# Kernel tuning notes

Measured on AMD Instinct MI355X. Metric: run time of the kernel, lower is better.

## Reference

```python
import jax, jax.numpy as jnp
import numpy as np

R = 32          # voxel_resolution
GN_GROUPS = 8   # GroupNorm groups used throughout the module


def group_norm(x, scale, bias, groups, eps=1e-5):
    B, C = x.shape[0], x.shape[1]
    spatial = x.shape[2:]
    xg = x.reshape(B, groups, C // groups, -1)
    mu = xg.mean(axis=(2, 3), keepdims=True)
    var = xg.var(axis=(2, 3), keepdims=True)
    xn = ((xg - mu) / jnp.sqrt(var + eps)).reshape((B, C) + spatial)
    sh = (1, C) + (1,) * len(spatial)
    return xn * scale.reshape(sh) + bias.reshape(sh)


def conv3d_same(x, w, b):
    pad = w.shape[-1] // 2
    y = jax.lax.conv_general_dilated(
        x, w, (1, 1, 1), [(pad, pad)] * 3,
        dimension_numbers=('NCDHW', 'OIDHW', 'NCDHW'))
    return y + b.reshape(1, -1, 1, 1, 1)


def _voxelize(coords, features, r):
    # PVCNN Voxelization: center coords, normalize to [0,1], scale to grid,
    # scatter-MEAN point features into a dense [B,C,r,r,r] grid.
    B, C, N = features.shape
    centered = coords - coords.mean(axis=2, keepdims=True)            # [B,3,N]
    norm = jnp.linalg.norm(centered, axis=1, keepdims=True)           # [B,1,N]
    denom = norm.max(axis=2, keepdims=True) * 2.0                     # eps = 0
    nc = centered / denom + 0.5
    nc = jnp.clip(nc * r, 0.0, r - 1.0)                               # float voxel coords
    vi = jnp.round(nc).astype(jnp.int32)                              # [B,3,N]
    flat = (vi[:, 0] * r + vi[:, 1]) * r + vi[:, 2]                   # [B,N]
    seg = (flat + (jnp.arange(B, dtype=jnp.int32) * (r ** 3))[:, None]).reshape(-1)
    feats = features.transpose(0, 2, 1).reshape(B * N, C)
    sums = jax.ops.segment_sum(feats, seg, num_segments=B * r ** 3)
    cnts = jax.ops.segment_sum(jnp.ones((B * N,), feats.dtype), seg,
                               num_segments=B * r ** 3)
    mean = sums / jnp.maximum(cnts, 1.0)[:, None]
    grid = mean.reshape(B, r, r, r, C).transpose(0, 4, 1, 2, 3)       # [B,C,r,r,r]
    return nc, grid


def _trilinear_devoxelize(nc, grid, r):
    # nc [B,3,N] float in [0,r-1]; grid [B,C,r,r,r] -> gather 8 corners + weights
    B, C = grid.shape[0], grid.shape[1]
    lo = jnp.floor(nc)
    frac = nc - lo                                                    # [B,3,N]
    lo_i = lo.astype(jnp.int32)
    hi_i = jnp.minimum(lo_i + 1, r - 1)
    gf = grid.reshape(B, C, r * r * r)
    out = jnp.zeros((B, C, nc.shape[2]), grid.dtype)
    for dx in (0, 1):
        for dy in (0, 1):
            for dz in (0, 1):
                ix = hi_i[:, 0] if dx else lo_i[:, 0]
                iy = hi_i[:, 1] if dy else lo_i[:, 1]
                iz = hi_i[:, 2] if dz else lo_i[:, 2]
                w = ((frac[:, 0] if dx else 1.0 - frac[:, 0]) *
                     (frac[:, 1] if dy else 1.0 - frac[:, 1]) *
                     (frac[:, 2] if dz else 1.0 - frac[:, 2]))        # [B,N]
                idx = (ix * r + iy) * r + iz                          # [B,N]
                g = jnp.take_along_axis(gf, idx[:, None, :], axis=2)  # [B,C,N]
                out = out + g * w[:, None, :]
    return out


def setup_inputs() -> dict:
    key = jax.random.key(0)
    ks = jax.random.split(key, 6)
    B, N, Cin, Cout, K = 4, 65536, 64, 128, 3
    return {
        'coords':   jax.random.normal(ks[0], (B, 3, N), jnp.float32),
        'features': jax.random.normal(ks[1], (B, Cin, N), jnp.float32),
        'conv1_w':  jax.random.normal(ks[2], (Cout, Cin, K, K, K), jnp.float32) * 0.02,
        'conv1_b':  jnp.zeros((Cout,), jnp.float32),
        'gn1_scale': jnp.ones((Cout,), jnp.float32),
        'gn1_bias':  jnp.zeros((Cout,), jnp.float32),
        'conv2_w':  jax.random.normal(ks[3], (Cout, Cout, K, K, K), jnp.float32) * 0.02,
        'conv2_b':  jnp.zeros((Cout,), jnp.float32),
        'gn2_scale': jnp.ones((Cout,), jnp.float32),
        'gn2_bias':  jnp.zeros((Cout,), jnp.float32),
        'point_w':  jax.random.normal(ks[4], (Cout, Cin), jnp.float32) * 0.05,
        'point_b':  jnp.zeros((Cout,), jnp.float32),
        'point_gn_scale': jnp.ones((Cout,), jnp.float32),
        'point_gn_bias':  jnp.zeros((Cout,), jnp.float32),
    }


def reference(coords, features, conv1_w, conv1_b, gn1_scale, gn1_bias,
              conv2_w, conv2_b, gn2_scale, gn2_bias,
              point_w, point_b, point_gn_scale, point_gn_bias):
    nc, grid = _voxelize(coords, features, R)
    # voxel branch: Conv3d -> GN -> SiLU -> (dropout, eval: identity) -> Conv3d -> GN -> SiLU
    h = conv3d_same(grid, conv1_w, conv1_b)
    h = jax.nn.silu(group_norm(h, gn1_scale, gn1_bias, GN_GROUPS))
    h = conv3d_same(h, conv2_w, conv2_b)
    h = jax.nn.silu(group_norm(h, gn2_scale, gn2_bias, GN_GROUPS))
    # point branch: SharedMLP = 1x1 Conv1d -> GN -> SiLU
    p = jnp.einsum('oc,bcn->bon', point_w, features) + point_b[None, :, None]
    p = jax.nn.silu(group_norm(p, point_gn_scale, point_gn_bias, GN_GROUPS))
    vpts = _trilinear_devoxelize(nc, h, R)                            # [B,Cout,N]
    return p + vpts
```

## Files before the change

### kernel.cpp

```cpp
#include <hip/hip_runtime.h>

typedef __attribute__((ext_vector_type(8))) short bf16x8;
typedef __attribute__((ext_vector_type(4))) float f32x4;
typedef __attribute__((ext_vector_type(4))) int i32x4;
typedef __attribute__((ext_vector_type(2))) int i32x2;

#define B_ 4
#define N_ 65536
#define RRR_ 32768
#define PADV_ 39304
#define PPLANE_ 1156

static const size_t OFF_NC     = 0;
static const size_t OFF_VIDX   = 786432;
static const size_t OFF_WT1    = 1048576;
static const size_t OFF_WT2    = 1159168;
static const size_t OFF_C2OUT  = 1380352;
static const size_t OFF_CNT    = 9768960;
static const size_t OFF_GSUM   = 9900032;
static const size_t OFF_GPAD   = 18288640;
static const size_t OFF_ACT1   = 23319552;
static const size_t OFF_GSTATS = 33381376;
static const size_t OFF_BSTATS = 33381568;
static const size_t MEMSET_FLOATS = 33381584 - 9768960;
static const size_t OFF_PBF    = 9900032;

__device__ __forceinline__ ushort f2bf(float x) {
    union { float f; unsigned u; } c; c.f = x;
    unsigned r = c.u + 0x7fffu + ((c.u >> 16) & 1u);
    return (ushort)(r >> 16);
}
__device__ __forceinline__ float bf2f(ushort h) {
    union { unsigned u; float f; } c; c.u = ((unsigned)h) << 16;
    return c.f;
}

__device__ __forceinline__ void gl16(const void* g, void* l) {
    __builtin_amdgcn_global_load_lds(
        (const __attribute__((address_space(1))) unsigned int*)(g),
        (__attribute__((address_space(3))) unsigned int*)(l),
        16, 0, 0);
}

__global__ __launch_bounds__(256) void k_coord_sum(const float* __restrict__ coords,
                                                   float* __restrict__ bstats) {
    int b = blockIdx.y;
    int tid = threadIdx.x;
    const float* cb = coords + (size_t)b * 3 * N_;
    float s0 = 0.f, s1 = 0.f, s2 = 0.f;
    for (int n = blockIdx.x * 256 + tid; n < N_; n += 64 * 256) {
        s0 += cb[n]; s1 += cb[N_ + n]; s2 += cb[2 * N_ + n];
    }
    #pragma unroll
    for (int off = 1; off < 64; off <<= 1) {
        s0 += __shfl_xor(s0, off);
        s1 += __shfl_xor(s1, off);
        s2 += __shfl_xor(s2, off);
    }
    if ((tid & 63) == 0) {
        atomicAdd(&bstats[b * 4 + 0], s0);
        atomicAdd(&bstats[b * 4 + 1], s1);
        atomicAdd(&bstats[b * 4 + 2], s2);
    }
}

__global__ __launch_bounds__(256) void k_coord_max(const float* __restrict__ coords,
                                                   float* __restrict__ bstats) {
    int b = blockIdx.y;
    int tid = threadIdx.x;
    const float invN = 1.0f / (float)N_;
    float m0 = bstats[b * 4 + 0] * invN;
    float m1 = bstats[b * 4 + 1] * invN;
    float m2 = bstats[b * 4 + 2] * invN;
    const float* cb = coords + (size_t)b * 3 * N_;
    float mx = 0.f;
    for (int n = blockIdx.x * 256 + tid; n < N_; n += 64 * 256) {
        float x = cb[n] - m0, y = cb[N_ + n] - m1, z = cb[2 * N_ + n] - m2;
        mx = fmaxf(mx, x * x + y * y + z * z);
    }
    #pragma unroll
    for (int off = 1; off < 64; off <<= 1)
        mx = fmaxf(mx, __shfl_xor(mx, off));
    if ((tid & 63) == 0)
        atomicMax((int*)&bstats[b * 4 + 3], __float_as_int(mx));
}

__global__ __launch_bounds__(256) void k_point_prep(const float* __restrict__ coords,
                                                    const float* __restrict__ bstats,
                                                    float* __restrict__ nc,
                                                    int* __restrict__ vidx,
                                                    float* __restrict__ cnt) {
    int gid = blockIdx.x * 256 + threadIdx.x;
    int b = gid >> 16;
    int n = gid & (N_ - 1);
    const float invN = 1.0f / (float)N_;
    float m[3] = {bstats[b * 4 + 0] * invN, bstats[b * 4 + 1] * invN, bstats[b * 4 + 2] * invN};
    float den = 2.0f * sqrtf(__int_as_float(((const int*)bstats)[b * 4 + 3]));
    const float* cb = coords + (size_t)b * 3 * N_;
    int vi[3];
    #pragma unroll
    for (int d = 0; d < 3; ++d) {
        float cv = cb[(size_t)d * N_ + n];
        float t = (cv - m[d]) / den + 0.5f;
        t *= 32.0f;
        t = fminf(fmaxf(t, 0.0f), 31.0f);
        nc[((size_t)b * 3 + d) * N_ + n] = t;
        vi[d] = (int)rintf(t);
    }
    int flat = (vi[0] * 32 + vi[1]) * 32 + vi[2];
    vidx[(b << 16) + n] = flat;
    atomicAdd(&cnt[(b << 15) + flat], 1.0f);
}

__global__ __launch_bounds__(256) void k_scatter_cl(const float* __restrict__ feats,
                                                    const int* __restrict__ vidx,
                                                    float* __restrict__ gsum) {
    __shared__ float lf[64 * 129];
    __shared__ int sidx[128];
    int tid = threadIdx.x;
    int b = blockIdx.y;
    int n0 = blockIdx.x * 128;
    for (int i = tid; i < 64 * 128; i += 256) {
        int ci = i >> 7, pt = i & 127;
        lf[ci * 129 + pt] = feats[((size_t)(b * 64 + ci)) * N_ + n0 + pt];
    }
    if (tid < 128) sidx[tid] = vidx[(b << 16) + n0 + tid];
    __syncthreads();
    for (int i = tid; i < 64 * 128; i += 256) {
        int ci = i & 63, pt = i >> 6;
        atomicAdd(&gsum[((size_t)(b << 15) + sidx[pt]) * 64 + ci], lf[ci * 129 + pt]);
    }
}

__global__ __launch_bounds__(256) void k_gridmean_cl(const float* __restrict__ gsum,
                                                     const float* __restrict__ cnt,
                                                     ushort* __restrict__ gpad) {
    int idx = blockIdx.x * 256 + threadIdx.x;
    int q = idx & 15;
    int vox = (idx >> 4) & 32767;
    int b = idx >> 19;
    float c = cnt[(b << 15) + vox];
    float inv = 1.0f / fmaxf(c, 1.0f);
    float4 v = *(const float4*)(gsum + (((size_t)(b << 15) + vox) << 6) + q * 4);
    int zz = vox >> 10, yy = (vox >> 5) & 31, xx = vox & 31;
    size_t o = ((size_t)b * PADV_ + (size_t)(zz + 1) * PPLANE_ + (yy + 1) * 34 + (xx + 1)) * 64 + q * 4;
    i32x2 pk;
    ushort* u = (ushort*)&pk;
    u[0] = f2bf(v.x * inv); u[1] = f2bf(v.y * inv);
    u[2] = f2bf(v.z * inv); u[3] = f2bf(v.w * inv);
    *(i32x2*)(gpad + o) = pk;
}

template <int CI>
__global__ __launch_bounds__(256) void k_wtrans(const float* __restrict__ w,
                                                ushort* __restrict__ wt) {
    int idx = blockIdx.x * 256 + threadIdx.x;
    if (idx >= 27 * 128 * CI) return;
    int chin = idx & 31;
    int co = (idx >> 5) & 127;
    int t3 = idx >> 12;
    int tap = t3 % 27;
    int chunk = t3 / 27;
    int ci = chunk * 32 + chin;
    wt[idx] = f2bf(w[((size_t)co * CI + ci) * 27 + tap]);
}

template <int CI, bool PAD_OUT>
__global__ __launch_bounds__(256, 3) void k_conv(const ushort* __restrict__ inp,
                                                 const ushort* __restrict__ wt,
                                                 const float* __restrict__ bias,
                                                 ushort* __restrict__ outp,
                                                 float* __restrict__ gstats,
                                                 int layer) {
    constexpr int NCHUNK = CI / 32;
    __shared__ char lds[40960];

    const int bid = blockIdx.x;
    const int wid = (bid & 7) * 128 + (bid >> 3);
    const int yg = wid & 7;
    const int z0 = (wid >> 3) & 31;
    const int b = wid >> 8;
    const int y0 = yg * 4;
    const int tid = threadIdx.x;
    const int w = tid >> 6, l = tid & 63;
    const int lk = l >> 4, lr = l & 15;
    const int wr = w >> 1, wc = w & 1;

    const char* actb = (const char*)(inp + (size_t)b * PADV_ * CI);
    const char* wtb = (const char*)wt;

    int st_glb[10];
    #pragma unroll
    for (int j = 0; j < 10; ++j) {
        int c = j * 64 + (tid >> 2);
        if (c > 611) c = 611;
        int row = c / 34;
        int x = c - row * 34;
        int dz = row / 6, dy = row - dz * 6;
        int gz = z0 + dz, gy = y0 + dy;
        int lq = (tid & 3) ^ ((x >> 1) & 3);
        st_glb[j] = (gz * PPLANE_ + gy * 34 + x) * CI * 2 + lq * 16;
    }

    int aoff[4][3];
    #pragma unroll
    for (int i = 0; i < 4; ++i) {
        int pos = wr * 64 + i * 16 + lr;
        int ly = pos >> 5, x = pos & 31;
        #pragma unroll
        for (int fx = 0; fx < 3; ++fx) {
            int xc = x + fx;
            aoff[i][fx] = (ly * 34 + xc) * 64 + ((lk ^ ((xc >> 1) & 3)) << 4);
        }
    }
    int bln[4];
    #pragma unroll
    for (int n = 0; n < 4; ++n)
        bln[n] = ((wc * 64 + n * 16 + lr) * 32 + lk * 8) * 2;

    f32x4 acc[4][4];
    #pragma unroll
    for (int i = 0; i < 4; ++i)
        #pragma unroll
        for (int n = 0; n < 4; ++n)
            acc[i][n] = (f32x4){0.f, 0.f, 0.f, 0.f};

    #pragma unroll 1
    for (int chunk = 0; chunk < NCHUNK; ++chunk) {
        __syncthreads();
        const char* wchunk = wtb + (size_t)chunk * 27 * 8192;
        bf16x8 bq[4][4];
        #pragma unroll
        for (int tp = 0; tp < 4; ++tp)
            #pragma unroll
            for (int n = 0; n < 4; ++n)
                bq[tp][n] = *(const bf16x8*)(wchunk + tp * 8192 + bln[n]);
        {
            const char* srcb = actb + chunk * 64;
            #pragma unroll
            for (int j = 0; j < 10; ++j)
                gl16(srcb + st_glb[j], lds + j * 4096 + w * 1024);
        }
        __syncthreads();

        #pragma unroll
        for (int t = 0; t < 27; ++t) {
            const int fz = t / 9, r9v = t - fz * 9;
            const int fy = r9v / 3, fx = r9v - fy * 3;
            const int drow = (fz * 6 + fy) * 2176;
            bf16x8 af[4];
            #pragma unroll
            for (int i = 0; i < 4; ++i)
                af[i] = *(const bf16x8*)(lds + drow + aoff[i][fx]);
            #pragma unroll
            for (int i = 0; i < 4; ++i)
                #pragma unroll
                for (int n = 0; n < 4; ++n)
                    acc[i][n] = __builtin_amdgcn_mfma_f32_16x16x32_bf16(af[i], bq[t & 3][n], acc[i][n], 0, 0, 0);
            if (t + 4 < 27) {
                const char* wp = wchunk + (size_t)(t + 4) * 8192;
                #pragma unroll
                for (int n = 0; n < 4; ++n) bq[t & 3][n] = *(const bf16x8*)(wp + bln[n]);
            }
        }
    }

    __syncthreads();
    ushort* outs = (ushort*)lds;
    float bb[4];
    #pragma unroll
    for (int n = 0; n < 4; ++n) bb[n] = bias[wc * 64 + n * 16 + lr];
    float sg[4] = {0.f, 0.f, 0.f, 0.f}, sq[4] = {0.f, 0.f, 0.f, 0.f};
    #pragma unroll
    for (int i = 0; i < 4; ++i) {
        int posb = wr * 64 + i * 16 + lk * 4;
        #pragma unroll
        for (int n = 0; n < 4; ++n) {
            int co = wc * 64 + n * 16 + lr;
            #pragma unroll
            for (int r = 0; r < 4; ++r) {
                float v = acc[i][n][r] + bb[n];
                sg[n] += v; sq[n] += v * v;
                outs[(posb + r) * 128 + co] = f2bf(v);
            }
        }
    }
    #pragma unroll
    for (int off = 1; off < 64; off <<= 1) {
        #pragma unroll
        for (int n = 0; n < 4; ++n) {
            sg[n] += __shfl_xor(sg[n], off);
            sq[n] += __shfl_xor(sq[n], off);
        }
    }
    if (l == 0) {
        int gbase = layer * 32 + b * 8 + wc * 4;
        #pragma unroll
        for (int n = 0; n < 4; ++n) {
            atomicAdd(&gstats[(gbase + n) * 2 + 0], sg[n]);
            atomicAdd(&gstats[(gbase + n) * 2 + 1], sq[n]);
        }
    }
    __syncthreads();
    for (int idx = tid; idx < 2048; idx += 256) {
        int pos = idx >> 4, c8 = idx & 15;
        int yy = y0 + (pos >> 5), xx = pos & 31;
        size_t g;
        if (PAD_OUT)
            g = ((size_t)b * PADV_ + (size_t)(z0 + 1) * PPLANE_ + (yy + 1) * 34 + (xx + 1)) * 128 + c8 * 8;
        else
            g = ((size_t)b * RRR_ + z0 * 1024 + yy * 32 + xx) * 128 + c8 * 8;
        *(i32x4*)(outp + g) = *((i32x4*)lds + idx);
    }
}

template <bool PAD>
__global__ __launch_bounds__(256) void k_gn_apply(ushort* __restrict__ x,
                                                  const float* __restrict__ gstats,
                                                  const float* __restrict__ sc,
                                                  const float* __restrict__ bi,
                                                  int layer, float invc) {
    int idx = blockIdx.x * 256 + threadIdx.x;
    int c8 = idx & 15;
    int vox = (idx >> 4) & 32767;
    int b = idx >> 19;
    size_t base;
    if (PAD) {
        int zz = vox >> 10, yy = (vox >> 5) & 31, xx = vox & 31;
        base = ((size_t)b * PADV_ + (size_t)(zz + 1) * PPLANE_ + (yy + 1) * 34 + (xx + 1)) * 128 + c8 * 8;
    } else {
        base = ((size_t)b * RRR_ + vox) * 128 + c8 * 8;
    }
    int g = c8 >> 1;
    float sum = gstats[(layer * 32 + b * 8 + g) * 2 + 0];
    float ssq = gstats[(layer * 32 + b * 8 + g) * 2 + 1];
    float mean = sum * invc;
    float var = ssq * invc - mean * mean;
    float rstd = rsqrtf(var + 1e-5f);
    i32x4 raw = *(i32x4*)(x + base);
    ushort* u = (ushort*)&raw;
    #pragma unroll
    for (int j = 0; j < 8; ++j) {
        int co = c8 * 8 + j;
        float v = bf2f(u[j]);
        v = (v - mean) * rstd * sc[co] + bi[co];
        v = v / (1.f + __expf(-v));
        u[j] = f2bf(v);
    }
    *(i32x4*)(x + base) = raw;
}

__global__ __launch_bounds__(256) void k_point_mlp(const float* __restrict__ feats,
                                                   const float* __restrict__ w,
                                                   const float* __restrict__ pb,
                                                   ushort* __restrict__ pbf,
                                                   float* __restrict__ gstats) {
    __shared__ float wl[64 * 132];
    __shared__ float sred[4][16];
    int tid = threadIdx.x;
    for (int i = tid; i < 128 * 64; i += 256) {
        int o = i >> 6, c = i & 63;
        wl[c * 132 + o] = w[i];
    }
    __syncthreads();
    int gid = blockIdx.x * 256 + tid;
    int b = gid >> 16, n = gid & (N_ - 1);
    const float* fb = feats + (size_t)b * 64 * N_ + n;
    float acc[128];
    #pragma unroll
    for (int o = 0; o < 128; ++o) acc[o] = 0.f;
    for (int c = 0; c < 64; ++c) {
        float f = fb[(size_t)c * N_];
        const float4* wr4 = (const float4*)&wl[c * 132];
        #pragma unroll
        for (int o4 = 0; o4 < 32; ++o4) {
            float4 wv = wr4[o4];
            acc[4 * o4 + 0] = fmaf(f, wv.x, acc[4 * o4 + 0]);
            acc[4 * o4 + 1] = fmaf(f, wv.y, acc[4 * o4 + 1]);
            acc[4 * o4 + 2] = fmaf(f, wv.z, acc[4 * o4 + 2]);
            acc[4 * o4 + 3] = fmaf(f, wv.w, acc[4 * o4 + 3]);
        }
    }
    ushort* ob = pbf + (size_t)b * 128 * N_ + n;
    float sg[8] = {0.f}, sq[8] = {0.f};
    #pragma unroll
    for (int o = 0; o < 128; ++o) {
        float v = acc[o] + pb[o];
        ob[(size_t)o * N_] = f2bf(v);
        sg[o >> 4] += v;
        sq[o >> 4] += v * v;
    }
    #pragma unroll
    for (int off = 1; off < 64; off <<= 1) {
        #pragma unroll
        for (int g = 0; g < 8; ++g) {
            sg[g] += __shfl_xor(sg[g], off);
            sq[g] += __shfl_xor(sq[g], off);
        }
    }
    int wv = tid >> 6, l = tid & 63;
    if (l == 0) {
        #pragma unroll
        for (int g = 0; g < 8; ++g) { sred[wv][g] = sg[g]; sred[wv][8 + g] = sq[g]; }
    }
    __syncthreads();
    if (tid < 16) {
        float v = sred[0][tid] + sred[1][tid] + sred[2][tid] + sred[3][tid];
        int g = tid & 7, part = tid >> 3;
        atomicAdd(&gstats[(64 + b * 8 + g) * 2 + part], v);
    }
}

__global__ __launch_bounds__(256) void k_devox_final(const float* __restrict__ nc,
                                                     const ushort* __restrict__ ht,
                                                     const ushort* __restrict__ pbf,
                                                     const float* __restrict__ gstats,
                                                     const float* __restrict__ scale,
                                                     const float* __restrict__ bias,
                                                     float* __restrict__ out) {
    __shared__ float vp[64][129];
    __shared__ int sidx[64][8];
    __shared__ float swt[64][8];
    int tid = threadIdx.x;
    int blk = blockIdx.x;
    int b = blk >> 10;
    int n0 = (blk & 1023) * 64;
    if (tid < 64) {
        int n = n0 + tid;
        float f0 = nc[(size_t)b * 3 * N_ + n];
        float f1 = nc[((size_t)b * 3 + 1) * N_ + n];
        float f2 = nc[((size_t)b * 3 + 2) * N_ + n];
        float l0 = floorf(f0), l1 = floorf(f1), l2 = floorf(f2);
        float r0 = f0 - l0, r1 = f1 - l1, r2 = f2 - l2;
        int i0 = (int)l0, i1 = (int)l1, i2 = (int)l2;
        int h0 = min(i0 + 1, 31), h1 = min(i1 + 1, 31), h2 = min(i2 + 1, 31);
        #pragma unroll
        for (int k = 0; k < 8; ++k) {
            int dx = (k >> 2) & 1, dy = (k >> 1) & 1, dz = k & 1;
            int ix = dx ? h0 : i0, iy = dy ? h1 : i1, iz = dz ? h2 : i2;
            float w = (dx ? r0 : 1.f - r0) * (dy ? r1 : 1.f - r1) * (dz ? r2 : 1.f - r2);
            sidx[tid][k] = (ix * 32 + iy) * 32 + iz;
            swt[tid][k] = w;
        }
    }
    __syncthreads();
    const ushort* hb = ht + (size_t)b * RRR_ * 128;
    for (int t = tid; t < 64 * 16; t += 256) {
        int c8 = t & 15, pt = t >> 4;
        float a[8] = {0.f, 0.f, 0.f, 0.f, 0.f, 0.f, 0.f, 0.f};
        #pragma unroll
        for (int k = 0; k < 8; ++k) {
            i32x4 raw = *(const i32x4*)(hb + (size_t)sidx[pt][k] * 128 + c8 * 8);
            ushort* u = (ushort*)&raw;
            float wk = swt[pt][k];
            #pragma unroll
            for (int j = 0; j < 8; ++j)
                a[j] = fmaf(wk, bf2f(u[j]), a[j]);
        }
        #pragma unroll
        for (int j = 0; j < 8; ++j)
            vp[pt][c8 * 8 + j] = a[j];
    }
    __syncthreads();
    const float invc = 1.0f / (16.0f * (float)N_);
    for (int t = tid; t < 64 * 128; t += 256) {
        int nl = t & 63;
        int c = t >> 6;
        int g = c >> 4;
        float sum = gstats[(64 + b * 8 + g) * 2 + 0];
        float ssq = gstats[(64 + b * 8 + g) * 2 + 1];
        float mean = sum * invc;
        float var = ssq * invc - mean * mean;
        float rstd = rsqrtf(var + 1e-5f);
        size_t o = ((size_t)(b * 128 + c)) * N_ + n0 + nl;
        float v = (bf2f(pbf[o]) - mean) * rstd * scale[c] + bias[c];
        v = v / (1.f + __expf(-v));
        out[o] = v + vp[nl][c];
    }
}

extern "C" void kernel_launch(void* const* d_in, const int* in_sizes, int n_in,
                              void* d_out, int out_size, void* d_ws, size_t ws_size,
                              hipStream_t stream) {
    const float* coords   = (const float*)d_in[0];
    const float* features = (const float*)d_in[1];
    const float* conv1_w  = (const float*)d_in[2];
    const float* conv1_b  = (const float*)d_in[3];
    const float* gn1_s    = (const float*)d_in[4];
    const float* gn1_b    = (const float*)d_in[5];
    const float* conv2_w  = (const float*)d_in[6];
    const float* conv2_b  = (const float*)d_in[7];
    const float* gn2_s    = (const float*)d_in[8];
    const float* gn2_b    = (const float*)d_in[9];
    const float* point_w  = (const float*)d_in[10];
    const float* point_b  = (const float*)d_in[11];
    const float* pgn_s    = (const float*)d_in[12];
    const float* pgn_b    = (const float*)d_in[13];
    float* out = (float*)d_out;
    float* ws = (float*)d_ws;

    float*  nc     = ws + OFF_NC;
    int*    vidx   = (int*)(ws + OFF_VIDX);
    ushort* wt1    = (ushort*)(ws + OFF_WT1);
    ushort* wt2    = (ushort*)(ws + OFF_WT2);
    ushort* c2out  = (ushort*)(ws + OFF_C2OUT);
    float*  cnt    = ws + OFF_CNT;
    float*  gsum   = ws + OFF_GSUM;
    ushort* gpad   = (ushort*)(ws + OFF_GPAD);
    ushort* act1   = (ushort*)(ws + OFF_ACT1);
    float*  gstats = ws + OFF_GSTATS;
    float*  bstats = ws + OFF_BSTATS;
    ushort* pbf    = (ushort*)(ws + OFF_PBF);

    const float invc = 1.0f / (float)(RRR_ * 16);

    hipMemsetAsync(cnt, 0, MEMSET_FLOATS * sizeof(float), stream);

    k_coord_sum<<<dim3(64, B_), 256, 0, stream>>>(coords, bstats);
    k_coord_max<<<dim3(64, B_), 256, 0, stream>>>(coords, bstats);
    k_point_prep<<<B_ * N_ / 256, 256, 0, stream>>>(coords, bstats, nc, vidx, cnt);
    k_scatter_cl<<<dim3(N_ / 128, B_), 256, 0, stream>>>(features, vidx, gsum);
    k_gridmean_cl<<<B_ * RRR_ * 16 / 256, 256, 0, stream>>>(gsum, cnt, gpad);

    k_wtrans<64><<<(27 * 128 * 64 + 255) / 256, 256, 0, stream>>>(conv1_w, wt1);
    k_wtrans<128><<<(27 * 128 * 128 + 255) / 256, 256, 0, stream>>>(conv2_w, wt2);

    k_conv<64, true><<<1024, 256, 0, stream>>>(gpad, wt1, conv1_b, act1, gstats, 0);
    k_gn_apply<true><<<B_ * RRR_ * 16 / 256, 256, 0, stream>>>(act1, gstats, gn1_s, gn1_b, 0, invc);

    k_conv<128, false><<<1024, 256, 0, stream>>>(act1, wt2, conv2_b, c2out, gstats, 1);
    k_gn_apply<false><<<B_ * RRR_ * 16 / 256, 256, 0, stream>>>(c2out, gstats, gn2_s, gn2_b, 1, invc);

    k_point_mlp<<<B_ * N_ / 256, 256, 0, stream>>>(features, point_w, point_b, pbf, gstats);
    k_devox_final<<<B_ * N_ / 64, 256, 0, stream>>>(nc, c2out, pbf, gstats, pgn_s, pgn_b, out);
}
```

Baseline: 1.036 ms.

## Stream conv weight taps through a swizzled LDS double-buffer ring with async loads

The conv kernel stops loading per-tap weight fragments from global memory into registers four taps ahead. Instead it stages each tap's weights into a two-slot LDS ring with async global-to-LDS copies, paced by explicit vmcnt waits and barriers, and uses setprio around the MFMA block. This is meant to cut register pressure and redundant global weight reads across waves, at the cost of more LDS, two barriers per tap and a lower occupancy hint (3 to 2). The devox kernel also remaps its block index to interleave batches.

Result: faster. 936.5 us (-9.6%).

```diff
diff --git a/kernel.cpp b/kernel.cpp
--- a/kernel.cpp
+++ b/kernel.cpp
@@ -166,14 +166,15 @@
 }
 
 template <int CI, bool PAD_OUT>
-__global__ __launch_bounds__(256, 3) void k_conv(const ushort* __restrict__ inp,
+__global__ __launch_bounds__(256, 2) void k_conv(const ushort* __restrict__ inp,
                                                  const ushort* __restrict__ wt,
                                                  const float* __restrict__ bias,
                                                  ushort* __restrict__ outp,
                                                  float* __restrict__ gstats,
                                                  int layer) {
     constexpr int NCHUNK = CI / 32;
-    __shared__ char lds[40960];
+    __shared__ char lds[40960 + 16384];
+    char* ring = lds + 40960;
 
     const int bid = blockIdx.x;
     const int wid = (bid & 7) * 128 + (bid >> 3);
@@ -201,7 +202,14 @@
         int lq = (tid & 3) ^ ((x >> 1) & 3);
         st_glb[j] = (gz * PPLANE_ + gy * 34 + x) * CI * 2 + lq * 16;
     }
-
+    int bst[2];
+    #pragma unroll
+    for (int i = 0; i < 2; ++i) {
+        int s = tid + i * 256;
+        int q = s & 3, co = s >> 2;
+        int sco = (co & 3) ^ ((co >> 2) & 3);
+        bst[i] = co * 64 + ((q ^ sco) << 4);
+    }
     int aoff[4][3];
     #pragma unroll
     for (int i = 0; i < 4; ++i) {
@@ -213,10 +221,13 @@
             aoff[i][fx] = (ly * 34 + xc) * 64 + ((lk ^ ((xc >> 1) & 3)) << 4);
         }
     }
-    int bln[4];
-    #pragma unroll
-    for (int n = 0; n < 4; ++n)
-        bln[n] = ((wc * 64 + n * 16 + lr) * 32 + lk * 8) * 2;
+    int boff[4];
+    #pragma unroll
+    for (int n = 0; n < 4; ++n) {
+        int co = wc * 64 + n * 16 + lr;
+        int sco = (co & 3) ^ ((co >> 2) & 3);
+        boff[n] = co * 64 + ((lk ^ sco) << 4);
+    }
 
     f32x4 acc[4][4];
     #pragma unroll
@@ -227,45 +238,60 @@
 
     #pragma unroll 1
     for (int chunk = 0; chunk < NCHUNK; ++chunk) {
-        __syncthreads();
-        const char* wchunk = wtb + (size_t)chunk * 27 * 8192;
-        bf16x8 bq[4][4];
-        #pragma unroll
-        for (int tp = 0; tp < 4; ++tp)
-            #pragma unroll
-            for (int n = 0; n < 4; ++n)
-                bq[tp][n] = *(const bf16x8*)(wchunk + tp * 8192 + bln[n]);
-        {
-            const char* srcb = actb + chunk * 64;
-            #pragma unroll
-            for (int j = 0; j < 10; ++j)
-                gl16(srcb + st_glb[j], lds + j * 4096 + w * 1024);
-        }
-        __syncthreads();
+        const char* srcb = actb + chunk * 64;
+        const char* wch = wtb + (size_t)chunk * 27 * 8192;
+        #pragma unroll
+        for (int j = 0; j < 10; ++j)
+            gl16(srcb + st_glb[j], lds + j * 4096 + w * 1024);
+        #pragma unroll
+        for (int i = 0; i < 2; ++i)
+            gl16(wch + bst[i], ring + i * 4096 + w * 1024);
+        #pragma unroll
+        for (int i = 0; i < 2; ++i)
+            gl16(wch + 8192 + bst[i], ring + 8192 + i * 4096 + w * 1024);
 
         #pragma unroll
         for (int t = 0; t < 27; ++t) {
+            __builtin_amdgcn_sched_barrier(0);
+            if (t == 26) {
+                asm volatile("s_waitcnt vmcnt(0)" ::: "memory");
+            } else {
+                asm volatile("s_waitcnt vmcnt(2)" ::: "memory");
+            }
+            __builtin_amdgcn_sched_barrier(0);
+            __builtin_amdgcn_s_barrier();
+            __builtin_amdgcn_sched_barrier(0);
+            const char* rp = ring + (t & 1) * 8192;
             const int fz = t / 9, r9v = t - fz * 9;
             const int fy = r9v / 3, fx = r9v - fy * 3;
             const int drow = (fz * 6 + fy) * 2176;
-            bf16x8 af[4];
+            bf16x8 af[4], bfr[4];
             #pragma unroll
             for (int i = 0; i < 4; ++i)
                 af[i] = *(const bf16x8*)(lds + drow + aoff[i][fx]);
             #pragma unroll
+            for (int n = 0; n < 4; ++n)
+                bfr[n] = *(const bf16x8*)(rp + boff[n]);
+            __builtin_amdgcn_s_setprio(1);
+            #pragma unroll
             for (int i = 0; i < 4; ++i)
                 #pragma unroll
                 for (int n = 0; n < 4; ++n)
-                    acc[i][n] = __builtin_amdgcn_mfma_f32_16x16x32_bf16(af[i], bq[t & 3][n], acc[i][n], 0, 0, 0);
-            if (t + 4 < 27) {
-                const char* wp = wchunk + (size_t)(t + 4) * 8192;
+                    acc[i][n] = __builtin_amdgcn_mfma_f32_16x16x32_bf16(af[i], bfr[n], acc[i][n], 0, 0, 0);
+            __builtin_amdgcn_s_setprio(0);
+            __builtin_amdgcn_sched_barrier(0);
+            __builtin_amdgcn_s_barrier();
+            __builtin_amdgcn_sched_barrier(0);
+            if (t + 2 < 27) {
+                const char* wp = wch + (size_t)(t + 2) * 8192;
+                char* rw = ring + (t & 1) * 8192;
                 #pragma unroll
-                for (int n = 0; n < 4; ++n) bq[t & 3][n] = *(const bf16x8*)(wp + bln[n]);
+                for (int i = 0; i < 2; ++i)
+                    gl16(wp + bst[i], rw + i * 4096 + w * 1024);
             }
         }
     }
 
-    __syncthreads();
     ushort* outs = (ushort*)lds;
     float bb[4];
     #pragma unroll
@@ -423,8 +449,9 @@
     __shared__ float swt[64][8];
     int tid = threadIdx.x;
     int blk = blockIdx.x;
-    int b = blk >> 10;
-    int n0 = (blk & 1023) * 64;
+    int wid = (blk & 7) * 512 + (blk >> 3);
+    int b = wid >> 10;
+    int n0 = (wid & 1023) * 64;
     if (tid < 64) {
         int n = n0 + tid;
         float f0 = nc[(size_t)b * 3 * N_ + n];
```
